# Kernel optimization log

Hardware: AMD Instinct MI355X
Metric: run time of the kernel (lower is better)

Reference implementation:

```python
import jax, jax.numpy as jnp
import numpy as np

N_NODES = 100000
N_FEATS = 256
OUT_DIM = 64
NNZ_X = 1280000
N_EDGES = 1600000
KEEP_PROB = 0.9  # 1 - dropout_rate (dropout_rate = 0.1)


def setup_inputs() -> dict:
    key = jax.random.key(0)
    ks = jax.random.split(key, 7)
    feat_values = jax.random.normal(ks[0], (NNZ_X,), dtype=jnp.float32)
    feat_rows = jax.random.randint(ks[1], (NNZ_X,), 0, N_NODES, dtype=jnp.int32)
    feat_cols = jax.random.randint(ks[2], (NNZ_X,), 0, N_FEATS, dtype=jnp.int32)
    # GlorotNormal kernel: std = sqrt(2 / (fan_in + fan_out))
    glorot_std = float(np.sqrt(2.0 / (N_FEATS + OUT_DIM)))
    kernel = jax.random.normal(ks[3], (N_FEATS, OUT_DIM), dtype=jnp.float32) * glorot_std
    adj_values = jax.random.uniform(ks[4], (N_EDGES,), dtype=jnp.float32)
    adj_rows = jax.random.randint(ks[5], (N_EDGES,), 0, N_NODES, dtype=jnp.int32)
    adj_cols = jax.random.randint(ks[6], (N_EDGES,), 0, N_NODES, dtype=jnp.int32)
    return {
        "feat_values": feat_values,
        "kernel": kernel,
        "adj_values": adj_values,
        "feat_rows": feat_rows,
        "feat_cols": feat_cols,
        "adj_rows": adj_rows,
        "adj_cols": adj_cols,
    }


def reference(feat_values, kernel, adj_values, feat_rows, feat_cols, adj_rows, adj_cols):
    # sparse dropout on feature values (training=True path), deterministic key.
    # tf: keep = floor(keep_prob + U[0,1)) cast to bool; retain then scale 1/keep_prob
    u = jax.random.uniform(jax.random.key(42), feat_values.shape, dtype=feat_values.dtype)
    keep = jnp.floor(KEEP_PROB + u).astype(bool)
    v = jnp.where(keep, feat_values, jnp.zeros_like(feat_values)) * (1.0 / KEEP_PROB)

    # SpMM 1: XW[n, o] = sum_{(n,f) in X} v * kernel[f, o]
    xw = jax.ops.segment_sum(v[:, None] * kernel[feat_cols], feat_rows,
                             num_segments=N_NODES)  # [N, OUT]

    # SpMM 2: out[i, o] = sum_{(i,j) in A} a_ij * xw[j, o]
    agg = jax.ops.segment_sum(adj_values[:, None] * xw[adj_cols], adj_rows,
                              num_segments=N_NODES)  # [N, OUT]

    return jax.nn.relu(agg)
```

## Files before the change

### kernel.cpp

```cpp
#include <hip/hip_runtime.h>

#define N_NODES 100000
#define N_FEATS 256
#define OUT_DIM 64
#define NNZ_X   1280000
#define N_EDGES 1600000
#define NB      391
#define CHUNK   4096
#define KPT     8
#define CAPX    4352
#define CAPA    5120

__device__ __forceinline__ unsigned rotl32(unsigned x, unsigned d) {
    return (x << d) | (x >> (32u - d));
}

__device__ __forceinline__ float jax_uniform_42(unsigned e) {
    unsigned x0 = 0u, x1 = e;
    const unsigned ks0 = 0u, ks1 = 42u, ks2 = 0u ^ 42u ^ 0x1BD11BDAu;
    x0 += ks0; x1 += ks1;
#define TF_R(r) { x0 += x1; x1 = rotl32(x1, r); x1 ^= x0; }
    TF_R(13) TF_R(15) TF_R(26) TF_R(6)
    x0 += ks1; x1 += ks2 + 1u;
    TF_R(17) TF_R(29) TF_R(16) TF_R(24)
    x0 += ks2; x1 += ks0 + 2u;
    TF_R(13) TF_R(15) TF_R(26) TF_R(6)
    x0 += ks0; x1 += ks1 + 3u;
    TF_R(17) TF_R(29) TF_R(16) TF_R(24)
    x0 += ks1; x1 += ks2 + 4u;
    TF_R(13) TF_R(15) TF_R(26) TF_R(6)
    x0 += ks2; x1 += ks0 + 5u;
#undef TF_R
    unsigned bits = x0 ^ x1;
    return __uint_as_float((bits >> 9) | 0x3f800000u) - 1.0f;
}

__device__ __forceinline__ bool keep_42(unsigned e) {
    float u = jax_uniform_42(e);
    return floorf(0.9f + u) != 0.0f;
}

__device__ __forceinline__ unsigned short f32_bf16(float f) {
    unsigned bits = __float_as_uint(f);
    return (unsigned short)((bits + 0x7fffu + ((bits >> 16) & 1u)) >> 16);
}

__device__ __forceinline__ float bflo(unsigned u) { return __uint_as_float(u << 16); }
__device__ __forceinline__ float bfhi(unsigned u) { return __uint_as_float(u & 0xffff0000u); }

__global__ __launch_bounds__(512) void phase1(
        const float* __restrict__ fvals, const int* __restrict__ frows,
        const int* __restrict__ fcols,
        const float* __restrict__ avals, const int* __restrict__ arows,
        const int* __restrict__ acols,
        int* __restrict__ bcur_x, int* __restrict__ bcur_a,
        float2* __restrict__ gx, float2* __restrict__ ga) {
    const int isA = blockIdx.y;
    const float* vals = isA ? avals : fvals;
    const int* rows   = isA ? arows : frows;
    const int* cols   = isA ? acols : fcols;
    int* bcur         = isA ? bcur_a : bcur_x;
    float2* dst       = isA ? ga : gx;
    const unsigned cap = isA ? CAPA : CAPX;
    const unsigned n  = isA ? N_EDGES : NNZ_X;

    unsigned t = threadIdx.x;
    unsigned base = blockIdx.x * CHUNK;
    if (base >= n) return;

    __shared__ int cnt[512];
    __shared__ int start[512];
    __shared__ int cur[512];
    __shared__ int gbase[NB];
    __shared__ int wtot[8];
    __shared__ int s_nvalid;
    __shared__ unsigned long long payload[CHUNK];
    __shared__ unsigned short bkt[CHUNK];

    int   rcache[KPT];
    float vcache[KPT];
    int   ccache[KPT];

    cnt[t] = 0;
    __syncthreads();
    #pragma unroll
    for (int k = 0; k < KPT; k++) {
        unsigned i = base + k * 512u + t;
        int r = -1;
        if (i < n) {
            int rr = rows[i];
            float v = vals[i];
            int   c = cols[i];
            if (isA || keep_42(i)) {
                r = rr;
                vcache[k] = isA ? v : v * (float)(1.0 / 0.9);
                ccache[k] = c;
            }
        }
        rcache[k] = r;
        if (r >= 0) atomicAdd(&cnt[(unsigned)r >> 8], 1);
    }
    __syncthreads();
    unsigned lane = t & 63u, wid = t >> 6;
    int binv = cnt[t];
    int inc = binv;
    #pragma unroll
    for (int d = 1; d < 64; d <<= 1) {
        int v = __shfl_up(inc, d, 64);
        if (lane >= (unsigned)d) inc += v;
    }
    if (lane == 63u) wtot[wid] = inc;
    __syncthreads();
    int offw = 0;
    #pragma unroll
    for (int w = 0; w < 8; w++) if ((unsigned)w < wid) offw += wtot[w];
    int excl = offw + inc - binv;
    start[t] = excl;
    cur[t]   = excl;
    if (t == 511u) s_nvalid = excl + binv;
    if (t < NB) {
        int cb = cnt[t];
        if (cb > 0) gbase[t] = atomicAdd(&bcur[t], cb);
    }
    __syncthreads();
    int n_valid = s_nvalid;
    #pragma unroll
    for (int k = 0; k < KPT; k++) {
        int r = rcache[k];
        if (r >= 0) {
            unsigned b = (unsigned)r >> 8;
            int p = atomicAdd(&cur[b], 1);
            unsigned packed = ((unsigned)ccache[k] << 8) | ((unsigned)r & 255u);
            payload[p] = ((unsigned long long)__float_as_uint(vcache[k]) << 32) | packed;
            bkt[p] = (unsigned short)b;
        }
    }
    __syncthreads();
    #pragma unroll
    for (int k = 0; k < KPT; k++) {
        int sidx = k * 512 + (int)t;
        if (sidx < n_valid) {
            unsigned b = bkt[sidx];
            unsigned long long m = payload[sidx];
            float2 e;
            e.x = __uint_as_float((unsigned)(m >> 32));
            e.y = __int_as_float((int)(unsigned)m);
            dst[(size_t)b * cap + gbase[b] + (sidx - start[b])] = e;
        }
    }
}

__global__ __launch_bounds__(1024) void sort_x_spmm1(
        const int* __restrict__ bcur_x, const float2* __restrict__ gx,
        const float* __restrict__ W, unsigned short* __restrict__ xw) {
    __shared__ float2 ent[CAPX];
    __shared__ int hist[256];
    __shared__ int starts[256];
    __shared__ int cursor[256];
    __shared__ int wtot[4];
    unsigned t = threadIdx.x;
    unsigned wid = t >> 6, lane = t & 63u;
    unsigned b = blockIdx.x;
    int cnt = bcur_x[b];
    const float2* src = gx + (size_t)b * CAPX;

    if (t < 256) hist[t] = 0;
    __syncthreads();
    float2 ec[4];
    #pragma unroll
    for (int k = 0; k < 4; k++) {
        int i = k * 1024 + (int)t;
        if (i < cnt) {
            float2 e = src[i];
            ec[k] = e;
            atomicAdd(&hist[((unsigned)__float_as_int(e.y)) & 255u], 1);
        }
    }
    for (int i = 4096 + (int)t; i < cnt; i += 1024)
        atomicAdd(&hist[((unsigned)__float_as_int(src[i].y)) & 255u], 1);
    __syncthreads();
    int inc = 0, binv = 0;
    if (wid < 4u) {
        unsigned bin = wid * 64u + lane;
        binv = hist[bin];
        inc = binv;
        #pragma unroll
        for (int d = 1; d < 64; d <<= 1) {
            int v = __shfl_up(inc, d, 64);
            if (lane >= (unsigned)d) inc += v;
        }
        if (lane == 63u) wtot[wid] = inc;
    }
    __syncthreads();
    if (wid < 4u) {
        int offw = 0;
        #pragma unroll
        for (int w = 0; w < 4; w++) if ((unsigned)w < wid) offw += wtot[w];
        unsigned bin = wid * 64u + lane;
        int excl = inc - binv + offw;
        starts[bin] = excl;
        cursor[bin] = excl;
    }
    __syncthreads();
    #pragma unroll
    for (int k = 0; k < 4; k++) {
        int i = k * 1024 + (int)t;
        if (i < cnt) {
            float2 e = ec[k];
            int pos = atomicAdd(&cursor[((unsigned)__float_as_int(e.y)) & 255u], 1);
            ent[pos] = e;
        }
    }
    for (int i = 4096 + (int)t; i < cnt; i += 1024) {
        float2 e = src[i];
        int pos = atomicAdd(&cursor[((unsigned)__float_as_int(e.y)) & 255u], 1);
        ent[pos] = e;
    }
    __syncthreads();
    unsigned quarter = lane >> 4, sub = lane & 15u;
    const float4* W4 = (const float4*)W;
    ushort4* xw4 = (ushort4*)xw;
    for (unsigned r = wid; r < 256u; r += 16u) {
        int s0 = starts[r];
        int s1 = (r == 255u) ? cnt : starts[r + 1];
        float4 acc[4];
        #pragma unroll
        for (int j = 0; j < 4; j++) { acc[j].x = acc[j].y = acc[j].z = acc[j].w = 0.0f; }
        int p = s0;
        for (; p + 16 <= s1; p += 16) {
            float2 e[4];
            #pragma unroll
            for (int j = 0; j < 4; j++) e[j] = ent[p + 4 * quarter + j];
            float4 w[4];
            #pragma unroll
            for (int j = 0; j < 4; j++)
                w[j] = W4[(((unsigned)__float_as_int(e[j].y)) >> 8) * 16u + sub];
            #pragma unroll
            for (int j = 0; j < 4; j++) {
                acc[j].x = fmaf(e[j].x, w[j].x, acc[j].x);
                acc[j].y = fmaf(e[j].x, w[j].y, acc[j].y);
                acc[j].z = fmaf(e[j].x, w[j].z, acc[j].z);
                acc[j].w = fmaf(e[j].x, w[j].w, acc[j].w);
            }
        }
        for (int q = p + (int)quarter; q < s1; q += 4) {
            float2 e = ent[q];
            float4 w = W4[(((unsigned)__float_as_int(e.y)) >> 8) * 16u + sub];
            acc[0].x = fmaf(e.x, w.x, acc[0].x);
            acc[0].y = fmaf(e.x, w.y, acc[0].y);
            acc[0].z = fmaf(e.x, w.z, acc[0].z);
            acc[0].w = fmaf(e.x, w.w, acc[0].w);
        }
        float ax = (acc[0].x + acc[1].x) + (acc[2].x + acc[3].x);
        float ay = (acc[0].y + acc[1].y) + (acc[2].y + acc[3].y);
        float az = (acc[0].z + acc[1].z) + (acc[2].z + acc[3].z);
        float aw = (acc[0].w + acc[1].w) + (acc[2].w + acc[3].w);
        ax += __shfl(ax, (int)(lane ^ 16u), 64);
        ay += __shfl(ay, (int)(lane ^ 16u), 64);
        az += __shfl(az, (int)(lane ^ 16u), 64);
        aw += __shfl(aw, (int)(lane ^ 16u), 64);
        ax += __shfl(ax, (int)(lane ^ 32u), 64);
        ay += __shfl(ay, (int)(lane ^ 32u), 64);
        az += __shfl(az, (int)(lane ^ 32u), 64);
        aw += __shfl(aw, (int)(lane ^ 32u), 64);
        unsigned grow = (b << 8) + r;
        if (quarter == 0 && grow < N_NODES) {
            ushort4 o;
            o.x = f32_bf16(ax); o.y = f32_bf16(ay);
            o.z = f32_bf16(az); o.w = f32_bf16(aw);
            xw4[(size_t)grow * 16u + sub] = o;
        }
    }
}

__global__ __launch_bounds__(1024) void sort_a_spmm2(
        const int* __restrict__ bcur_a, const float2* __restrict__ ga,
        const unsigned short* __restrict__ xw, float* __restrict__ out) {
    __shared__ float2 ent[CAPA];
    __shared__ int hist[256];
    __shared__ int starts[256];
    __shared__ int cursor[256];
    __shared__ int wtot[4];
    unsigned t = threadIdx.x;
    unsigned wid = t >> 6, lane = t & 63u;
    unsigned b = blockIdx.x;
    int cnt = bcur_a[b];
    const float2* src = ga + (size_t)b * CAPA;

    if (t < 256) hist[t] = 0;
    __syncthreads();
    float2 ec[5];
    #pragma unroll
    for (int k = 0; k < 5; k++) {
        int i = k * 1024 + (int)t;
        if (i < cnt) {
            float2 e = src[i];
            ec[k] = e;
            atomicAdd(&hist[((unsigned)__float_as_int(e.y)) & 255u], 1);
        }
    }
    __syncthreads();
    int inc = 0, binv = 0;
    if (wid < 4u) {
        unsigned bin = wid * 64u + lane;
        binv = hist[bin];
        inc = binv;
        #pragma unroll
        for (int d = 1; d < 64; d <<= 1) {
            int v = __shfl_up(inc, d, 64);
            if (lane >= (unsigned)d) inc += v;
        }
        if (lane == 63u) wtot[wid] = inc;
    }
    __syncthreads();
    if (wid < 4u) {
        int offw = 0;
        #pragma unroll
        for (int w = 0; w < 4; w++) if ((unsigned)w < wid) offw += wtot[w];
        unsigned bin = wid * 64u + lane;
        int excl = inc - binv + offw;
        starts[bin] = excl;
        cursor[bin] = excl;
    }
    __syncthreads();
    #pragma unroll
    for (int k = 0; k < 5; k++) {
        int i = k * 1024 + (int)t;
        if (i < cnt) {
            float2 e = ec[k];
            int pos = atomicAdd(&cursor[((unsigned)__float_as_int(e.y)) & 255u], 1);
            ent[pos] = e;
        }
    }
    __syncthreads();
    unsigned oct = lane >> 3, sub = lane & 7u;
    const uint4* xw8 = (const uint4*)xw;
    for (unsigned r = wid; r < 256u; r += 16u) {
        int s0 = starts[r];
        int s1 = (r == 255u) ? cnt : starts[r + 1];
        float acc[8];
        #pragma unroll
        for (int j = 0; j < 8; j++) acc[j] = 0.0f;
        int p = s0 + (int)oct;
        for (; p + 8 < s1; p += 16) {
            float2 e0 = ent[p];
            float2 e1 = ent[p + 8];
            uint4 u0 = xw8[(((unsigned)__float_as_int(e0.y)) >> 8) * 8u + sub];
            uint4 u1 = xw8[(((unsigned)__float_as_int(e1.y)) >> 8) * 8u + sub];
            float v0 = e0.x, v1 = e1.x;
            acc[0] = fmaf(v0, bflo(u0.x), acc[0]);
            acc[1] = fmaf(v0, bfhi(u0.x), acc[1]);
            acc[2] = fmaf(v0, bflo(u0.y), acc[2]);
            acc[3] = fmaf(v0, bfhi(u0.y), acc[3]);
            acc[4] = fmaf(v0, bflo(u0.z), acc[4]);
            acc[5] = fmaf(v0, bfhi(u0.z), acc[5]);
            acc[6] = fmaf(v0, bflo(u0.w), acc[6]);
            acc[7] = fmaf(v0, bfhi(u0.w), acc[7]);
            acc[0] = fmaf(v1, bflo(u1.x), acc[0]);
            acc[1] = fmaf(v1, bfhi(u1.x), acc[1]);
            acc[2] = fmaf(v1, bflo(u1.y), acc[2]);
            acc[3] = fmaf(v1, bfhi(u1.y), acc[3]);
            acc[4] = fmaf(v1, bflo(u1.z), acc[4]);
            acc[5] = fmaf(v1, bfhi(u1.z), acc[5]);
            acc[6] = fmaf(v1, bflo(u1.w), acc[6]);
            acc[7] = fmaf(v1, bfhi(u1.w), acc[7]);
        }
        if (p < s1) {
            float2 e = ent[p];
            uint4 u = xw8[(((unsigned)__float_as_int(e.y)) >> 8) * 8u + sub];
            float v = e.x;
            acc[0] = fmaf(v, bflo(u.x), acc[0]);
            acc[1] = fmaf(v, bfhi(u.x), acc[1]);
            acc[2] = fmaf(v, bflo(u.y), acc[2]);
            acc[3] = fmaf(v, bfhi(u.y), acc[3]);
            acc[4] = fmaf(v, bflo(u.z), acc[4]);
            acc[5] = fmaf(v, bfhi(u.z), acc[5]);
            acc[6] = fmaf(v, bflo(u.w), acc[6]);
            acc[7] = fmaf(v, bfhi(u.w), acc[7]);
        }
        #pragma unroll
        for (int j = 0; j < 8; j++) {
            acc[j] += __shfl_xor(acc[j], 8, 64);
            acc[j] += __shfl_xor(acc[j], 16, 64);
            acc[j] += __shfl_xor(acc[j], 32, 64);
        }
        unsigned grow = (b << 8) + r;
        if (oct == 0 && grow < N_NODES) {
            float4 o0, o1;
            o0.x = fmaxf(acc[0], 0.0f);
            o0.y = fmaxf(acc[1], 0.0f);
            o0.z = fmaxf(acc[2], 0.0f);
            o0.w = fmaxf(acc[3], 0.0f);
            o1.x = fmaxf(acc[4], 0.0f);
            o1.y = fmaxf(acc[5], 0.0f);
            o1.z = fmaxf(acc[6], 0.0f);
            o1.w = fmaxf(acc[7], 0.0f);
            float4* op = (float4*)(out + (size_t)grow * 64u + sub * 8u);
            op[0] = o0;
            op[1] = o1;
        }
    }
}

extern "C" void kernel_launch(void* const* d_in, const int* in_sizes, int n_in,
                              void* d_out, int out_size, void* d_ws, size_t ws_size,
                              hipStream_t stream) {
    const float* feat_values = (const float*)d_in[0];
    const float* W           = (const float*)d_in[1];
    const float* adj_values  = (const float*)d_in[2];
    const int*   feat_rows   = (const int*)d_in[3];
    const int*   feat_cols   = (const int*)d_in[4];
    const int*   adj_rows    = (const int*)d_in[5];
    const int*   adj_cols    = (const int*)d_in[6];
    float* out = (float*)d_out;

    char* ws = (char*)d_ws;
    int* bcur_x = (int*)(ws + 0);
    int* bcur_a = (int*)(ws + 2048);
    float2* gx  = (float2*)(ws + 204800);
    float2* ga  = (float2*)(ws + 13817856);
    unsigned short* xw = (unsigned short*)(ws + 29833216);

    hipMemsetAsync(ws, 0, 4096, stream);

    dim3 gp1((N_EDGES + CHUNK - 1) / CHUNK, 2);
    phase1<<<gp1, 512, 0, stream>>>(feat_values, feat_rows, feat_cols,
                                    adj_values, adj_rows, adj_cols,
                                    bcur_x, bcur_a, gx, ga);
    sort_x_spmm1<<<NB, 1024, 0, stream>>>(bcur_x, gx, W, xw);
    sort_a_spmm2<<<NB, 1024, 0, stream>>>(bcur_a, ga, xw, out);
}
```

Baseline: 179.9 us.

## Split each row bucket across two half-blocks of 512 threads

Each 256-row bucket is now handled by two 512-thread blocks, and each block keeps only the entries whose row bit 7 matches its half. Grid size doubles and per-block shared memory roughly halves. The aim is more blocks in flight across CUs and less shared memory per block, so occupancy and load balance improve. Every block still reads the whole bucket from global memory, so bucket reads double. The x kernel also drops its overflow loop for counts above the register cache, now capped at 9*512 entries.

New measurement: 181.1 us. About the same (+0.7%).

```diff
diff --git a/kernel.cpp b/kernel.cpp
--- a/kernel.cpp
+++ b/kernel.cpp
@@ -10,6 +10,8 @@
 #define KPT     8
 #define CAPX    4352
 #define CAPA    5120
+#define CAPXH   2560
+#define CAPAH   3072
 
 __device__ __forceinline__ unsigned rotl32(unsigned x, unsigned d) {
     return (x << d) | (x >> (32u - d));
@@ -150,37 +152,40 @@
     }
 }
 
-__global__ __launch_bounds__(1024) void sort_x_spmm1(
+__global__ __launch_bounds__(512) void sort_x_spmm1(
         const int* __restrict__ bcur_x, const float2* __restrict__ gx,
         const float* __restrict__ W, unsigned short* __restrict__ xw) {
-    __shared__ float2 ent[CAPX];
-    __shared__ int hist[256];
-    __shared__ int starts[256];
-    __shared__ int cursor[256];
-    __shared__ int wtot[4];
+    __shared__ float2 ent[CAPXH];
+    __shared__ int hist[128];
+    __shared__ int starts[128];
+    __shared__ int cursor[128];
+    __shared__ int wtot[2];
     unsigned t = threadIdx.x;
     unsigned wid = t >> 6, lane = t & 63u;
-    unsigned b = blockIdx.x;
+    unsigned b = blockIdx.x >> 1, h = blockIdx.x & 1u;
     int cnt = bcur_x[b];
     const float2* src = gx + (size_t)b * CAPX;
 
-    if (t < 256) hist[t] = 0;
-    __syncthreads();
-    float2 ec[4];
-    #pragma unroll
-    for (int k = 0; k < 4; k++) {
-        int i = k * 1024 + (int)t;
+    if (t < 128) hist[t] = 0;
+    __syncthreads();
+    float2 ec[9];
+    unsigned mineMask = 0;
+    #pragma unroll
+    for (int k = 0; k < 9; k++) {
+        int i = k * 512 + (int)t;
         if (i < cnt) {
             float2 e = src[i];
             ec[k] = e;
-            atomicAdd(&hist[((unsigned)__float_as_int(e.y)) & 255u], 1);
-        }
-    }
-    for (int i = 4096 + (int)t; i < cnt; i += 1024)
-        atomicAdd(&hist[((unsigned)__float_as_int(src[i].y)) & 255u], 1);
+            unsigned pk = (unsigned)__float_as_int(e.y);
+            if (((pk >> 7) & 1u) == h) {
+                mineMask |= (1u << k);
+                atomicAdd(&hist[pk & 127u], 1);
+            }
+        }
+    }
     __syncthreads();
     int inc = 0, binv = 0;
-    if (wid < 4u) {
+    if (wid < 2u) {
         unsigned bin = wid * 64u + lane;
         binv = hist[bin];
         inc = binv;
@@ -192,37 +197,29 @@
         if (lane == 63u) wtot[wid] = inc;
     }
     __syncthreads();
-    if (wid < 4u) {
-        int offw = 0;
-        #pragma unroll
-        for (int w = 0; w < 4; w++) if ((unsigned)w < wid) offw += wtot[w];
+    if (wid < 2u) {
         unsigned bin = wid * 64u + lane;
-        int excl = inc - binv + offw;
+        int excl = inc - binv + (wid == 1u ? wtot[0] : 0);
         starts[bin] = excl;
         cursor[bin] = excl;
     }
     __syncthreads();
     #pragma unroll
-    for (int k = 0; k < 4; k++) {
-        int i = k * 1024 + (int)t;
-        if (i < cnt) {
+    for (int k = 0; k < 9; k++) {
+        if ((mineMask >> k) & 1u) {
             float2 e = ec[k];
-            int pos = atomicAdd(&cursor[((unsigned)__float_as_int(e.y)) & 255u], 1);
+            int pos = atomicAdd(&cursor[((unsigned)__float_as_int(e.y)) & 127u], 1);
             ent[pos] = e;
         }
     }
-    for (int i = 4096 + (int)t; i < cnt; i += 1024) {
-        float2 e = src[i];
-        int pos = atomicAdd(&cursor[((unsigned)__float_as_int(e.y)) & 255u], 1);
-        ent[pos] = e;
-    }
-    __syncthreads();
+    __syncthreads();
+    int cntH = wtot[0] + wtot[1];
     unsigned quarter = lane >> 4, sub = lane & 15u;
     const float4* W4 = (const float4*)W;
     ushort4* xw4 = (ushort4*)xw;
-    for (unsigned r = wid; r < 256u; r += 16u) {
+    for (unsigned r = wid; r < 128u; r += 8u) {
         int s0 = starts[r];
-        int s1 = (r == 255u) ? cnt : starts[r + 1];
+        int s1 = (r == 127u) ? cntH : starts[r + 1];
         float4 acc[4];
         #pragma unroll
         for (int j = 0; j < 4; j++) { acc[j].x = acc[j].y = acc[j].z = acc[j].w = 0.0f; }
@@ -263,7 +260,7 @@
         ay += __shfl(ay, (int)(lane ^ 32u), 64);
         az += __shfl(az, (int)(lane ^ 32u), 64);
         aw += __shfl(aw, (int)(lane ^ 32u), 64);
-        unsigned grow = (b << 8) + r;
+        unsigned grow = (b << 8) + (h << 7) + r;
         if (quarter == 0 && grow < N_NODES) {
             ushort4 o;
             o.x = f32_bf16(ax); o.y = f32_bf16(ay);
@@ -273,35 +270,40 @@
     }
 }
 
-__global__ __launch_bounds__(1024) void sort_a_spmm2(
+__global__ __launch_bounds__(512) void sort_a_spmm2(
         const int* __restrict__ bcur_a, const float2* __restrict__ ga,
         const unsigned short* __restrict__ xw, float* __restrict__ out) {
-    __shared__ float2 ent[CAPA];
-    __shared__ int hist[256];
-    __shared__ int starts[256];
-    __shared__ int cursor[256];
-    __shared__ int wtot[4];
+    __shared__ float2 ent[CAPAH];
+    __shared__ int hist[128];
+    __shared__ int starts[128];
+    __shared__ int cursor[128];
+    __shared__ int wtot[2];
     unsigned t = threadIdx.x;
     unsigned wid = t >> 6, lane = t & 63u;
-    unsigned b = blockIdx.x;
+    unsigned b = blockIdx.x >> 1, h = blockIdx.x & 1u;
     int cnt = bcur_a[b];
     const float2* src = ga + (size_t)b * CAPA;
 
-    if (t < 256) hist[t] = 0;
-    __syncthreads();
-    float2 ec[5];
-    #pragma unroll
-    for (int k = 0; k < 5; k++) {
-        int i = k * 1024 + (int)t;
+    if (t < 128) hist[t] = 0;
+    __syncthreads();
+    float2 ec[10];
+    unsigned mineMask = 0;
+    #pragma unroll
+    for (int k = 0; k < 10; k++) {
+        int i = k * 512 + (int)t;
         if (i < cnt) {
             float2 e = src[i];
             ec[k] = e;
-            atomicAdd(&hist[((unsigned)__float_as_int(e.y)) & 255u], 1);
+            unsigned pk = (unsigned)__float_as_int(e.y);
+            if (((pk >> 7) & 1u) == h) {
+                mineMask |= (1u << k);
+                atomicAdd(&hist[pk & 127u], 1);
+            }
         }
     }
     __syncthreads();
     int inc = 0, binv = 0;
-    if (wid < 4u) {
+    if (wid < 2u) {
         unsigned bin = wid * 64u + lane;
         binv = hist[bin];
         inc = binv;
@@ -313,31 +315,28 @@
         if (lane == 63u) wtot[wid] = inc;
     }
     __syncthreads();
-    if (wid < 4u) {
-        int offw = 0;
-        #pragma unroll
-        for (int w = 0; w < 4; w++) if ((unsigned)w < wid) offw += wtot[w];
+    if (wid < 2u) {
         unsigned bin = wid * 64u + lane;
-        int excl = inc - binv + offw;
+        int excl = inc - binv + (wid == 1u ? wtot[0] : 0);
         starts[bin] = excl;
         cursor[bin] = excl;
     }
     __syncthreads();
     #pragma unroll
-    for (int k = 0; k < 5; k++) {
-        int i = k * 1024 + (int)t;
-        if (i < cnt) {
+    for (int k = 0; k < 10; k++) {
+        if ((mineMask >> k) & 1u) {
             float2 e = ec[k];
-            int pos = atomicAdd(&cursor[((unsigned)__float_as_int(e.y)) & 255u], 1);
+            int pos = atomicAdd(&cursor[((unsigned)__float_as_int(e.y)) & 127u], 1);
             ent[pos] = e;
         }
     }
     __syncthreads();
+    int cntH = wtot[0] + wtot[1];
     unsigned oct = lane >> 3, sub = lane & 7u;
     const uint4* xw8 = (const uint4*)xw;
-    for (unsigned r = wid; r < 256u; r += 16u) {
+    for (unsigned r = wid; r < 128u; r += 8u) {
         int s0 = starts[r];
-        int s1 = (r == 255u) ? cnt : starts[r + 1];
+        int s1 = (r == 127u) ? cntH : starts[r + 1];
         float acc[8];
         #pragma unroll
         for (int j = 0; j < 8; j++) acc[j] = 0.0f;
@@ -384,7 +383,7 @@
             acc[j] += __shfl_xor(acc[j], 16, 64);
             acc[j] += __shfl_xor(acc[j], 32, 64);
         }
-        unsigned grow = (b << 8) + r;
+        unsigned grow = (b << 8) + (h << 7) + r;
         if (oct == 0 && grow < N_NODES) {
             float4 o0, o1;
             o0.x = fmaxf(acc[0], 0.0f);
@@ -427,6 +426,6 @@
     phase1<<<gp1, 512, 0, stream>>>(feat_values, feat_rows, feat_cols,
                                     adj_values, adj_rows, adj_cols,
                                     bcur_x, bcur_a, gx, ga);
-    sort_x_spmm1<<<NB, 1024, 0, stream>>>(bcur_x, gx, W, xw);
-    sort_a_spmm2<<<NB, 1024, 0, stream>>>(bcur_a, ga, xw, out);
-}
+    sort_x_spmm1<<<2 * NB, 512, 0, stream>>>(bcur_x, gx, W, xw);
+    sort_a_spmm2<<<2 * NB, 512, 0, stream>>>(bcur_a, ga, xw, out);
+}
```
